# Kernel tuning notes

Hardware: AMD Instinct MI355X
Metric: run time of the kernel (lower is better)

Reference implementation:

```python
import jax, jax.numpy as jnp
import numpy as np

H = 64  # hidden_size
F = 32  # input_size
B, T = 4096, 256


def setup_inputs() -> dict:
    key = jax.random.key(0)
    ks = jax.random.split(key, 12)
    s = 1.0 / np.sqrt(H)  # torch LSTM init scale
    u = lambda k, shape: jax.random.uniform(k, shape, jnp.float32, -s, s)
    return {
        "x": jax.random.normal(ks[0], (B, T, F), jnp.float32),
        # layer 0 (input_size=F)
        "W_ih0": u(ks[1], (4 * H, F)),
        "W_hh0": u(ks[2], (4 * H, H)),
        "b_ih0": u(ks[3], (4 * H,)),
        "b_hh0": u(ks[4], (4 * H,)),
        # layer 1 (input_size=H)
        "W_ih1": u(ks[5], (4 * H, H)),
        "W_hh1": u(ks[6], (4 * H, H)),
        "b_ih1": u(ks[7], (4 * H,)),
        "b_hh1": u(ks[8], (4 * H,)),
        # linear head
        "W_out": u(ks[9], (1, H)),
        "b_out": u(ks[10], (1,)),
    }


def _lstm_layer(x, W_ih, W_hh, b_ih, b_hh):
    # x: [B, T, D] -> hidden sequence [B, T, H]; PyTorch gate order i,f,g,o.
    b = x.shape[0]
    h_dim = W_hh.shape[1]
    # precompute input contribution for all timesteps: [B, T, 4H]
    gx = jnp.einsum('btd,gd->btg', x, W_ih) + b_ih + b_hh

    def step(carry, g_t):
        h, c = carry
        g = g_t + h @ W_hh.T  # [B, 4H]
        i, f, gg, o = jnp.split(g, 4, axis=-1)
        c = jax.nn.sigmoid(f) * c + jax.nn.sigmoid(i) * jnp.tanh(gg)
        h = jax.nn.sigmoid(o) * jnp.tanh(c)
        return (h, c), h

    h0 = jnp.zeros((b, h_dim), x.dtype)
    (_, _), hs = jax.lax.scan(step, (h0, h0), jnp.swapaxes(gx, 0, 1))
    return jnp.swapaxes(hs, 0, 1)  # [B, T, H]


def reference(x, W_ih0, W_hh0, b_ih0, b_hh0, W_ih1, W_hh1, b_ih1, b_hh1, W_out, b_out):
    h = _lstm_layer(x, W_ih0, W_hh0, b_ih0, b_hh0)
    h = _lstm_layer(h, W_ih1, W_hh1, b_ih1, b_hh1)
    last = h[:, -1, :]  # [B, H]; dropout is identity at inference
    return last @ W_out.T + b_out  # [B, 1]
```

## Files before the change

### kernel.cpp

```cpp
#include <hip/hip_runtime.h>

typedef _Float16 half8 __attribute__((ext_vector_type(8)));
typedef float f32x4 __attribute__((ext_vector_type(4)));

#define T_STEPS 256
#define NB      16
#define NBLOCKS (4096/NB)
#define LOG2E   1.4426950408889634f

#define SH 136

__device__ __forceinline__ half8 cvt8s(const float* __restrict__ p, float s) {
    half8 r;
    #pragma unroll
    for (int j = 0; j < 8; ++j) r[j] = (_Float16)(p[j] * s);
    return r;
}

__device__ __forceinline__ void sync_lds() {
    asm volatile("s_waitcnt lgkmcnt(0)" ::: "memory");
    __builtin_amdgcn_s_barrier();
}

__global__ __launch_bounds__(1024, 4)
void lstm_v12(const float* __restrict__ x,
              const float* __restrict__ Wih0, const float* __restrict__ Whh0,
              const float* __restrict__ bih0, const float* __restrict__ bhh0,
              const float* __restrict__ Wih1, const float* __restrict__ Whh1,
              const float* __restrict__ bih1, const float* __restrict__ bhh1,
              const float* __restrict__ Wout, const float* __restrict__ bout,
              float* __restrict__ out)
{
    __shared__ _Float16 Hb[2][16][SH];

    const int tid  = threadIdx.x;
    const int w    = tid >> 6;
    const bool isL1 = (w < 8);
    const int wq   = w & 7;
    const int l    = tid & 63;
    const int ln   = l & 15;
    const int lb   = l >> 4;
    const int U0   = 8 * wq;
    const int gb0  = blockIdx.x * NB;

    const int qa = ln & 3;
    const int ua = ln >> 2;
    const float sa = (qa == 2) ? 2.f * LOG2E : -LOG2E;

    half8 wa[2][4];
    f32x4 bv[2];
    if (isL1) {
        #pragma unroll
        for (int t = 0; t < 2; ++t) {
            const int gr = 64 * qa + U0 + 4 * t + ua;
            wa[t][0] = cvt8s(Wih0 + gr * 32 + 8 * lb, sa);
            wa[t][1] = cvt8s(Whh0 + gr * 64 + 8 * lb, sa);
            wa[t][2] = cvt8s(Whh0 + gr * 64 + 32 + 8 * lb, sa);
            #pragma unroll
            for (int jj = 0; jj < 4; ++jj) {
                const int g = 64 * jj + U0 + 4 * t + lb;
                const float s = (jj == 2) ? 2.f * LOG2E : -LOG2E;
                bv[t][jj] = (bih0[g] + bhh0[g]) * s;
            }
        }
    } else {
        #pragma unroll
        for (int t = 0; t < 2; ++t) {
            const int gr = 64 * qa + U0 + 4 * t + ua;
            #pragma unroll
            for (int ks = 0; ks < 4; ++ks) {
                const int c0 = 32 * ks + 8 * lb;
                const float* p = (c0 < 64) ? (Wih1 + gr * 64 + c0)
                                           : (Whh1 + gr * 64 + (c0 - 64));
                wa[t][ks] = cvt8s(p, sa);
            }
            #pragma unroll
            for (int jj = 0; jj < 4; ++jj) {
                const int g = 64 * jj + U0 + 4 * t + lb;
                const float s = (jj == 2) ? 2.f * LOG2E : -LOG2E;
                bv[t][jj] = (bih1[g] + bhh1[g]) * s;
            }
        }
    }

    float cst0 = 0.f, cst1 = 0.f;

    {
        unsigned int* z = (unsigned int*)Hb;
        for (int i = tid; i < (int)(sizeof(Hb) / 4); i += 1024) z[i] = 0u;
    }

    const float* xb = x + (long)(gb0 + ln) * T_STEPS * 32 + 8 * lb;
    f32x4 xr0 = {0.f,0.f,0.f,0.f}, xr1 = {0.f,0.f,0.f,0.f};
    f32x4 gxA[2], gxB[2];
    if (isL1) {
        const f32x4 x0a = *(const f32x4*)(xb);
        const f32x4 x0b = *(const f32x4*)(xb + 4);
        half8 xf;
        #pragma unroll
        for (int j = 0; j < 4; ++j) { xf[j] = (_Float16)x0a[j]; xf[4+j] = (_Float16)x0b[j]; }
        gxA[0] = __builtin_amdgcn_mfma_f32_16x16x32_f16(wa[0][0], xf, bv[0], 0, 0, 0);
        gxA[1] = __builtin_amdgcn_mfma_f32_16x16x32_f16(wa[1][0], xf, bv[1], 0, 0, 0);
        xr0 = *(const f32x4*)(xb + 32);
        xr1 = *(const f32x4*)(xb + 36);
    }
    sync_lds();

#define ACT_U(AV, CS, HOUT)                                                    \
    {                                                                          \
        const float ei = __builtin_amdgcn_exp2f(AV[0]);                        \
        const float ef = __builtin_amdgcn_exp2f(AV[1]);                        \
        const float Eg = __builtin_amdgcn_exp2f(AV[2]);                        \
        const float eo = __builtin_amdgcn_exp2f(AV[3]);                        \
        const float ti = 1.f + ei, tf = 1.f + ef, tg = 1.f + Eg;               \
        const float pig = ti * tg;                                             \
        const float num = fmaf(Eg - 1.f, tf, (CS) * pig);                      \
        const float c   = num * __builtin_amdgcn_rcpf(pig * tf);               \
        (CS) = c;                                                              \
        const float Ec  = __builtin_amdgcn_exp2f(fminf((2.f * LOG2E) * c, 120.f)); \
        HOUT = (_Float16)((Ec - 1.f) *                                         \
               __builtin_amdgcn_rcpf((1.f + eo) * (1.f + Ec)));                \
    }

#define STEP(J, P, GXC, GXN)                                                   \
    do {                                                                       \
        if (isL1 && (J) < T_STEPS) {                                           \
            const half8 bf0 = *(const half8*)&Hb[P][ln][8 * lb];               \
            const half8 bf1 = *(const half8*)&Hb[P][ln][32 + 8 * lb];          \
            half8 xf;                                                          \
            _Pragma("unroll")                                                  \
            for (int j = 0; j < 4; ++j) { xf[j] = (_Float16)xr0[j]; xf[4+j] = (_Float16)xr1[j]; } \
            GXN[0] = __builtin_amdgcn_mfma_f32_16x16x32_f16(wa[0][0], xf, bv[0], 0, 0, 0); \
            GXN[1] = __builtin_amdgcn_mfma_f32_16x16x32_f16(wa[1][0], xf, bv[1], 0, 0, 0); \
            { const int jn = ((J) + 2 < T_STEPS) ? (J) + 2 : T_STEPS - 1;      \
              xr0 = *(const f32x4*)(xb + jn * 32);                             \
              xr1 = *(const f32x4*)(xb + jn * 32 + 4); }                       \
            __builtin_amdgcn_s_setprio(1);                                     \
            GXC[0] = __builtin_amdgcn_mfma_f32_16x16x32_f16(wa[0][1], bf0, GXC[0], 0, 0, 0); \
            GXC[1] = __builtin_amdgcn_mfma_f32_16x16x32_f16(wa[1][1], bf0, GXC[1], 0, 0, 0); \
            GXC[0] = __builtin_amdgcn_mfma_f32_16x16x32_f16(wa[0][2], bf1, GXC[0], 0, 0, 0); \
            GXC[1] = __builtin_amdgcn_mfma_f32_16x16x32_f16(wa[1][2], bf1, GXC[1], 0, 0, 0); \
            __builtin_amdgcn_s_setprio(0);                                     \
            _Float16 h0v, h1v;                                                 \
            ACT_U(GXC[0], cst0, h0v) ACT_U(GXC[1], cst1, h1v)                  \
            Hb[1 - (P)][ln][U0 + lb]     = h0v;                                \
            Hb[1 - (P)][ln][U0 + 4 + lb] = h1v;                                \
        }                                                                      \
        if (!isL1 && (J) >= 1 && (J) <= T_STEPS) {                             \
            const half8 bf0 = *(const half8*)&Hb[P][ln][8 * lb];               \
            const half8 bf1 = *(const half8*)&Hb[P][ln][32 + 8 * lb];          \
            const half8 bf2 = *(const half8*)&Hb[P][ln][64 + 8 * lb];          \
            const half8 bf3 = *(const half8*)&Hb[P][ln][96 + 8 * lb];          \
            f32x4 a0 = bv[0], a1 = bv[1];                                      \
            __builtin_amdgcn_s_setprio(1);                                     \
            a0 = __builtin_amdgcn_mfma_f32_16x16x32_f16(wa[0][0], bf0, a0, 0, 0, 0); \
            a1 = __builtin_amdgcn_mfma_f32_16x16x32_f16(wa[1][0], bf0, a1, 0, 0, 0); \
            a0 = __builtin_amdgcn_mfma_f32_16x16x32_f16(wa[0][1], bf1, a0, 0, 0, 0); \
            a1 = __builtin_amdgcn_mfma_f32_16x16x32_f16(wa[1][1], bf1, a1, 0, 0, 0); \
            a0 = __builtin_amdgcn_mfma_f32_16x16x32_f16(wa[0][2], bf2, a0, 0, 0, 0); \
            a1 = __builtin_amdgcn_mfma_f32_16x16x32_f16(wa[1][2], bf2, a1, 0, 0, 0); \
            a0 = __builtin_amdgcn_mfma_f32_16x16x32_f16(wa[0][3], bf3, a0, 0, 0, 0); \
            a1 = __builtin_amdgcn_mfma_f32_16x16x32_f16(wa[1][3], bf3, a1, 0, 0, 0); \
            __builtin_amdgcn_s_setprio(0);                                     \
            _Float16 h0v, h1v;                                                 \
            ACT_U(a0, cst0, h0v) ACT_U(a1, cst1, h1v)                          \
            Hb[1 - (P)][ln][64 + U0 + lb]     = h0v;                           \
            Hb[1 - (P)][ln][64 + U0 + 4 + lb] = h1v;                           \
        }                                                                      \
        sync_lds();                                                            \
    } while (0)

    for (int jj = 0; jj < T_STEPS; jj += 2) {
        STEP(jj, 0, gxA, gxB);
        STEP(jj + 1, 1, gxB, gxA);
    }
    STEP(T_STEPS, 0, gxA, gxB);

    if (tid < NB) {
        float s = bout[0];
        #pragma unroll
        for (int u8 = 0; u8 < 8; ++u8) {
            const half8 hv = *(const half8*)&Hb[1][tid][64 + 8 * u8];
            #pragma unroll
            for (int j = 0; j < 8; ++j)
                s += (float)hv[j] * Wout[8 * u8 + j];
        }
        out[gb0 + tid] = s;
    }
}

extern "C" void kernel_launch(void* const* d_in, const int* in_sizes, int n_in,
                              void* d_out, int out_size, void* d_ws, size_t ws_size,
                              hipStream_t stream) {
    const float* x    = (const float*)d_in[0];
    const float* Wih0 = (const float*)d_in[1];
    const float* Whh0 = (const float*)d_in[2];
    const float* bih0 = (const float*)d_in[3];
    const float* bhh0 = (const float*)d_in[4];
    const float* Wih1 = (const float*)d_in[5];
    const float* Whh1 = (const float*)d_in[6];
    const float* bih1 = (const float*)d_in[7];
    const float* bhh1 = (const float*)d_in[8];
    const float* Wout = (const float*)d_in[9];
    const float* bout = (const float*)d_in[10];

    hipLaunchKernelGGL(lstm_v12, dim3(NBLOCKS), dim3(1024), 0, stream,
                       x, Wih0, Whh0, bih0, bhh0,
                       Wih1, Whh1, bih1, bhh1, Wout, bout,
                       (float*)d_out);
}
```

Measured before the change: 181.1 us.

## Merge layer-1 and layer-2 waves so each wave computes both LSTM layers

Halves the block to 8 waves, with each wave now handling the same 8 hidden units of both layers per step instead of splitting layers across separate wave groups. All weights for both layers are kept in registers, and the shared LDS hidden-state reads are loaded once and reused by both layers' MFMAs. This aims to reduce barrier participants per block and allow more independent blocks per CU, at the cost of more serial MFMA and activation work per wave per step, higher register pressure, and removal of the priority hints.

```diff
diff --git a/kernel.cpp b/kernel.cpp
--- a/kernel.cpp
+++ b/kernel.cpp
@@ -22,8 +22,8 @@
     __builtin_amdgcn_s_barrier();
 }
 
-__global__ __launch_bounds__(1024, 4)
-void lstm_v12(const float* __restrict__ x,
+__global__ __launch_bounds__(512, 2)
+void lstm_v13(const float* __restrict__ x,
               const float* __restrict__ Wih0, const float* __restrict__ Whh0,
               const float* __restrict__ bih0, const float* __restrict__ bhh0,
               const float* __restrict__ Wih1, const float* __restrict__ Whh1,
@@ -33,74 +33,59 @@
 {
     __shared__ _Float16 Hb[2][16][SH];
 
-    const int tid  = threadIdx.x;
-    const int w    = tid >> 6;
-    const bool isL1 = (w < 8);
-    const int wq   = w & 7;
-    const int l    = tid & 63;
-    const int ln   = l & 15;
-    const int lb   = l >> 4;
-    const int U0   = 8 * wq;
-    const int gb0  = blockIdx.x * NB;
+    const int tid = threadIdx.x;
+    const int w   = tid >> 6;
+    const int l   = tid & 63;
+    const int ln  = l & 15;
+    const int lb  = l >> 4;
+    const int U0  = 8 * w;
+    const int gb0 = blockIdx.x * NB;
 
     const int qa = ln & 3;
     const int ua = ln >> 2;
     const float sa = (qa == 2) ? 2.f * LOG2E : -LOG2E;
 
-    half8 wa[2][4];
-    f32x4 bv[2];
-    if (isL1) {
+    half8 wa1[2][3];
+    half8 wa2[2][4];
+    f32x4 bv1[2], bv2[2];
+    #pragma unroll
+    for (int t = 0; t < 2; ++t) {
+        const int gr = 64 * qa + U0 + 4 * t + ua;
+        wa1[t][0] = cvt8s(Wih0 + gr * 32 + 8 * lb, sa);
+        wa1[t][1] = cvt8s(Whh0 + gr * 64 + 8 * lb, sa);
+        wa1[t][2] = cvt8s(Whh0 + gr * 64 + 32 + 8 * lb, sa);
+        wa2[t][0] = cvt8s(Wih1 + gr * 64 + 8 * lb, sa);
+        wa2[t][1] = cvt8s(Wih1 + gr * 64 + 32 + 8 * lb, sa);
+        wa2[t][2] = cvt8s(Whh1 + gr * 64 + 8 * lb, sa);
+        wa2[t][3] = cvt8s(Whh1 + gr * 64 + 32 + 8 * lb, sa);
         #pragma unroll
-        for (int t = 0; t < 2; ++t) {
-            const int gr = 64 * qa + U0 + 4 * t + ua;
-            wa[t][0] = cvt8s(Wih0 + gr * 32 + 8 * lb, sa);
-            wa[t][1] = cvt8s(Whh0 + gr * 64 + 8 * lb, sa);
-            wa[t][2] = cvt8s(Whh0 + gr * 64 + 32 + 8 * lb, sa);
-            #pragma unroll
-            for (int jj = 0; jj < 4; ++jj) {
-                const int g = 64 * jj + U0 + 4 * t + lb;
-                const float s = (jj == 2) ? 2.f * LOG2E : -LOG2E;
-                bv[t][jj] = (bih0[g] + bhh0[g]) * s;
-            }
-        }
-    } else {
-        #pragma unroll
-        for (int t = 0; t < 2; ++t) {
-            const int gr = 64 * qa + U0 + 4 * t + ua;
-            #pragma unroll
-            for (int ks = 0; ks < 4; ++ks) {
-                const int c0 = 32 * ks + 8 * lb;
-                const float* p = (c0 < 64) ? (Wih1 + gr * 64 + c0)
-                                           : (Whh1 + gr * 64 + (c0 - 64));
-                wa[t][ks] = cvt8s(p, sa);
-            }
-            #pragma unroll
-            for (int jj = 0; jj < 4; ++jj) {
-                const int g = 64 * jj + U0 + 4 * t + lb;
-                const float s = (jj == 2) ? 2.f * LOG2E : -LOG2E;
-                bv[t][jj] = (bih1[g] + bhh1[g]) * s;
-            }
+        for (int jj = 0; jj < 4; ++jj) {
+            const int g = 64 * jj + U0 + 4 * t + lb;
+            const float s = (jj == 2) ? 2.f * LOG2E : -LOG2E;
+            bv1[t][jj] = (bih0[g] + bhh0[g]) * s;
+            bv2[t][jj] = (bih1[g] + bhh1[g]) * s;
         }
     }
 
-    float cst0 = 0.f, cst1 = 0.f;
+    float c1a = 0.f, c1b = 0.f;
+    float c2a = 0.f, c2b = 0.f;
 
     {
         unsigned int* z = (unsigned int*)Hb;
-        for (int i = tid; i < (int)(sizeof(Hb) / 4); i += 1024) z[i] = 0u;
+        for (int i = tid; i < (int)(sizeof(Hb) / 4); i += 512) z[i] = 0u;
     }
 
     const float* xb = x + (long)(gb0 + ln) * T_STEPS * 32 + 8 * lb;
-    f32x4 xr0 = {0.f,0.f,0.f,0.f}, xr1 = {0.f,0.f,0.f,0.f};
+    f32x4 xr0, xr1;
     f32x4 gxA[2], gxB[2];
-    if (isL1) {
+    {
         const f32x4 x0a = *(const f32x4*)(xb);
         const f32x4 x0b = *(const f32x4*)(xb + 4);
         half8 xf;
         #pragma unroll
         for (int j = 0; j < 4; ++j) { xf[j] = (_Float16)x0a[j]; xf[4+j] = (_Float16)x0b[j]; }
-        gxA[0] = __builtin_amdgcn_mfma_f32_16x16x32_f16(wa[0][0], xf, bv[0], 0, 0, 0);
-        gxA[1] = __builtin_amdgcn_mfma_f32_16x16x32_f16(wa[1][0], xf, bv[1], 0, 0, 0);
+        gxA[0] = __builtin_amdgcn_mfma_f32_16x16x32_f16(wa1[0][0], xf, bv1[0], 0, 0, 0);
+        gxA[1] = __builtin_amdgcn_mfma_f32_16x16x32_f16(wa1[1][0], xf, bv1[1], 0, 0, 0);
         xr0 = *(const f32x4*)(xb + 32);
         xr1 = *(const f32x4*)(xb + 36);
     }
@@ -124,46 +109,48 @@
 
 #define STEP(J, P, GXC, GXN)                                                   \
     do {                                                                       \
-        if (isL1 && (J) < T_STEPS) {                                           \
-            const half8 bf0 = *(const half8*)&Hb[P][ln][8 * lb];               \
-            const half8 bf1 = *(const half8*)&Hb[P][ln][32 + 8 * lb];          \
+         \
+        const half8 f10 = *(const half8*)&Hb[P][ln][8 * lb];                   \
+        const half8 f11 = *(const half8*)&Hb[P][ln][32 + 8 * lb];              \
+        const half8 f20 = *(const half8*)&Hb[P][ln][64 + 8 * lb];              \
+        const half8 f21 = *(const half8*)&Hb[P][ln][96 + 8 * lb];              \
+             \
+        if ((J) < T_STEPS) {                                                   \
             half8 xf;                                                          \
             _Pragma("unroll")                                                  \
             for (int j = 0; j < 4; ++j) { xf[j] = (_Float16)xr0[j]; xf[4+j] = (_Float16)xr1[j]; } \
-            GXN[0] = __builtin_amdgcn_mfma_f32_16x16x32_f16(wa[0][0], xf, bv[0], 0, 0, 0); \
-            GXN[1] = __builtin_amdgcn_mfma_f32_16x16x32_f16(wa[1][0], xf, bv[1], 0, 0, 0); \
-            { const int jn = ((J) + 2 < T_STEPS) ? (J) + 2 : T_STEPS - 1;      \
-              xr0 = *(const f32x4*)(xb + jn * 32);                             \
-              xr1 = *(const f32x4*)(xb + jn * 32 + 4); }                       \
-            __builtin_amdgcn_s_setprio(1);                                     \
-            GXC[0] = __builtin_amdgcn_mfma_f32_16x16x32_f16(wa[0][1], bf0, GXC[0], 0, 0, 0); \
-            GXC[1] = __builtin_amdgcn_mfma_f32_16x16x32_f16(wa[1][1], bf0, GXC[1], 0, 0, 0); \
-            GXC[0] = __builtin_amdgcn_mfma_f32_16x16x32_f16(wa[0][2], bf1, GXC[0], 0, 0, 0); \
-            GXC[1] = __builtin_amdgcn_mfma_f32_16x16x32_f16(wa[1][2], bf1, GXC[1], 0, 0, 0); \
-            __builtin_amdgcn_s_setprio(0);                                     \
+            GXN[0] = __builtin_amdgcn_mfma_f32_16x16x32_f16(wa1[0][0], xf, bv1[0], 0, 0, 0); \
+            GXN[1] = __builtin_amdgcn_mfma_f32_16x16x32_f16(wa1[1][0], xf, bv1[1], 0, 0, 0); \
+            const int jn = ((J) + 2 < T_STEPS) ? (J) + 2 : T_STEPS - 1;        \
+            xr0 = *(const f32x4*)(xb + jn * 32);                               \
+            xr1 = *(const f32x4*)(xb + jn * 32 + 4);                           \
+        }                                                                      \
+                                  \
+        f32x4 a20, a21;                                                        \
+        if ((J) >= 1) {                                                        \
+            a20 = __builtin_amdgcn_mfma_f32_16x16x32_f16(wa2[0][0], f10, bv2[0], 0, 0, 0); \
+            a21 = __builtin_amdgcn_mfma_f32_16x16x32_f16(wa2[1][0], f10, bv2[1], 0, 0, 0); \
+            a20 = __builtin_amdgcn_mfma_f32_16x16x32_f16(wa2[0][1], f11, a20, 0, 0, 0); \
+            a21 = __builtin_amdgcn_mfma_f32_16x16x32_f16(wa2[1][1], f11, a21, 0, 0, 0); \
+            a20 = __builtin_amdgcn_mfma_f32_16x16x32_f16(wa2[0][2], f20, a20, 0, 0, 0); \
+            a21 = __builtin_amdgcn_mfma_f32_16x16x32_f16(wa2[1][2], f20, a21, 0, 0, 0); \
+            a20 = __builtin_amdgcn_mfma_f32_16x16x32_f16(wa2[0][3], f21, a20, 0, 0, 0); \
+            a21 = __builtin_amdgcn_mfma_f32_16x16x32_f16(wa2[1][3], f21, a21, 0, 0, 0); \
+        }                                                                      \
+              \
+        if ((J) < T_STEPS) {                                                   \
+            GXC[0] = __builtin_amdgcn_mfma_f32_16x16x32_f16(wa1[0][1], f10, GXC[0], 0, 0, 0); \
+            GXC[1] = __builtin_amdgcn_mfma_f32_16x16x32_f16(wa1[1][1], f10, GXC[1], 0, 0, 0); \
+            GXC[0] = __builtin_amdgcn_mfma_f32_16x16x32_f16(wa1[0][2], f11, GXC[0], 0, 0, 0); \
+            GXC[1] = __builtin_amdgcn_mfma_f32_16x16x32_f16(wa1[1][2], f11, GXC[1], 0, 0, 0); \
             _Float16 h0v, h1v;                                                 \
-            ACT_U(GXC[0], cst0, h0v) ACT_U(GXC[1], cst1, h1v)                  \
+            ACT_U(GXC[0], c1a, h0v) ACT_U(GXC[1], c1b, h1v)                    \
             Hb[1 - (P)][ln][U0 + lb]     = h0v;                                \
             Hb[1 - (P)][ln][U0 + 4 + lb] = h1v;                                \
         }                                                                      \
-        if (!isL1 && (J) >= 1 && (J) <= T_STEPS) {                             \
-            const half8 bf0 = *(const half8*)&Hb[P][ln][8 * lb];               \
-            const half8 bf1 = *(const half8*)&Hb[P][ln][32 + 8 * lb];          \
-            const half8 bf2 = *(const half8*)&Hb[P][ln][64 + 8 * lb];          \
-            const half8 bf3 = *(const half8*)&Hb[P][ln][96 + 8 * lb];          \
-            f32x4 a0 = bv[0], a1 = bv[1];                                      \
-            __builtin_amdgcn_s_setprio(1);                                     \
-            a0 = __builtin_amdgcn_mfma_f32_16x16x32_f16(wa[0][0], bf0, a0, 0, 0, 0); \
-            a1 = __builtin_amdgcn_mfma_f32_16x16x32_f16(wa[1][0], bf0, a1, 0, 0, 0); \
-            a0 = __builtin_amdgcn_mfma_f32_16x16x32_f16(wa[0][1], bf1, a0, 0, 0, 0); \
-            a1 = __builtin_amdgcn_mfma_f32_16x16x32_f16(wa[1][1], bf1, a1, 0, 0, 0); \
-            a0 = __builtin_amdgcn_mfma_f32_16x16x32_f16(wa[0][2], bf2, a0, 0, 0, 0); \
-            a1 = __builtin_amdgcn_mfma_f32_16x16x32_f16(wa[1][2], bf2, a1, 0, 0, 0); \
-            a0 = __builtin_amdgcn_mfma_f32_16x16x32_f16(wa[0][3], bf3, a0, 0, 0, 0); \
-            a1 = __builtin_amdgcn_mfma_f32_16x16x32_f16(wa[1][3], bf3, a1, 0, 0, 0); \
-            __builtin_amdgcn_s_setprio(0);                                     \
+        if ((J) >= 1) {                                                        \
             _Float16 h0v, h1v;                                                 \
-            ACT_U(a0, cst0, h0v) ACT_U(a1, cst1, h1v)                          \
+            ACT_U(a20, c2a, h0v) ACT_U(a21, c2b, h1v)                          \
             Hb[1 - (P)][ln][64 + U0 + lb]     = h0v;                           \
             Hb[1 - (P)][ln][64 + U0 + 4 + lb] = h1v;                           \
         }                                                                      \
@@ -204,7 +191,7 @@
     const float* Wout = (const float*)d_in[9];
     const float* bout = (const float*)d_in[10];
 
-    hipLaunchKernelGGL(lstm_v12, dim3(NBLOCKS), dim3(1024), 0, stream,
+    hipLaunchKernelGGL(lstm_v13, dim3(NBLOCKS), dim3(512), 0, stream,
                        x, Wih0, Whh0, bih0, bhh0,
                        Wih1, Whh1, bih1, bhh1, Wout, bout,
                        (float*)d_out);
```

Result: no change. 183.4 us (+1.2%).
